# Optimization experiments

Hardware: AMD Instinct MI355X
Metric: run time of the kernel (lower is better)

The kernel has to match this reference:

```python
import jax, jax.numpy as jnp
import numpy as np

N_EDGES = 1_600_000
N_NODES = 50_000
D_FEAT = 32


def setup_inputs() -> dict:
    key = jax.random.key(0)
    k_src, k_idx = jax.random.split(key)
    src = jax.random.normal(k_src, (N_EDGES, D_FEAT), dtype=jnp.float32)
    index = jax.random.randint(k_idx, (N_EDGES,), 0, N_NODES, dtype=jnp.int64 if jax.config.jax_enable_x64 else jnp.int32)
    out = jnp.zeros((N_NODES, D_FEAT), dtype=jnp.float32)
    return {"src": src, "index": index, "out": out}


def reference(src, index, out):
    # scatter_add(src, index, dim=0, out=out): out[index[e], :] += src[e, :]
    # Equivalent to out + segment_sum over the edge dim.
    return out + jax.ops.segment_sum(src, index, num_segments=out.shape[0])
```

## Files before the change

### kernel.cpp

```cpp
#include <hip/hip_runtime.h>

#define N_EDGES 1600000
#define N_NODES 50000
#define D_FEAT  32

#define BSHIFT  6
#define NPB     64
#define NB      ((N_NODES + NPB - 1) / NPB)
#define CHUNK   4096
#define NBLK    ((N_EDGES + CHUNK - 1) / CHUNK)
#define EPT     (CHUNK / 256)

#define BLKCNT_OFF 0
#define START_OFF  ((((size_t)NBLK * NB * 4 + 255) / 256) * 256)
#define PB_OFF     (START_OFF + ((((size_t)(NB + 1) * 4 + 255) / 256) * 256))
#define OFFS_OFF   (PB_OFF + (size_t)N_EDGES * 4)
#define PERM_OFF   (OFFS_OFF + ((((size_t)(N_NODES + 1) * 4 + 255) / 256) * 256))
#define WS_NEEDED  (PERM_OFF + (size_t)N_EDGES * 4)

__global__ __launch_bounds__(256) void count_kernel(const int* __restrict__ index,
                                                    int* __restrict__ blockcnt) {
    __shared__ int lcnt[NB];
    int t = threadIdx.x;
    for (int k = t; k < NB; k += 256) lcnt[k] = 0;
    __syncthreads();
    int base = blockIdx.x * CHUNK;
    #pragma unroll
    for (int j = 0; j < EPT; ++j) {
        int e = base + j * 256 + t;
        if (e < N_EDGES) atomicAdd(&lcnt[index[e] >> BSHIFT], 1);
    }
    __syncthreads();
    for (int k = t; k < NB; k += 256)
        blockcnt[(size_t)blockIdx.x * NB + k] = lcnt[k];
}

__global__ __launch_bounds__(256) void scan_col_kernel(int* __restrict__ blockcnt,
                                                       int* __restrict__ startg) {
    int wid  = (blockIdx.x * 256 + threadIdx.x) >> 6;
    int lane = threadIdx.x & 63;
    if (wid >= NB) return;
    int carry = 0;
    const int CH = (NBLK + 63) / 64;
    for (int c = 0; c < CH; ++c) {
        int b = c * 64 + lane;
        int v = (b < NBLK) ? blockcnt[(size_t)b * NB + wid] : 0;
        int incl = v;
        #pragma unroll
        for (int d = 1; d < 64; d <<= 1) {
            int up = __shfl_up(incl, d, 64);
            if (lane >= d) incl += up;
        }
        if (b < NBLK) blockcnt[(size_t)b * NB + wid] = carry + incl - v;
        carry += __shfl(incl, 63, 64);
    }
    if (lane == 0) startg[wid] = carry;
}

__global__ __launch_bounds__(1024) void scan_bucket_kernel(int* __restrict__ startg) {
    __shared__ int part[1024];
    int t = threadIdx.x;
    int v = (t < NB) ? startg[t] : 0;
    part[t] = v;
    __syncthreads();
    int inc = v;
    for (int d = 1; d < 1024; d <<= 1) {
        int w = (t >= d) ? part[t - d] : 0;
        __syncthreads();
        inc += w;
        part[t] = inc;
        __syncthreads();
    }
    if (t < NB) startg[t] = inc - v;
    if (t == 0) startg[NB] = N_EDGES;
}

__global__ __launch_bounds__(256) void partition_kernel(const int* __restrict__ index,
                                                        const int* __restrict__ blockcnt,
                                                        const int* __restrict__ startg,
                                                        int* __restrict__ pb) {
    __shared__ int lcnt[NB];
    __shared__ int loff[NB];
    __shared__ int lbase[NB];
    __shared__ int scanp[256];
    __shared__ int2 stage[CHUNK];
    int t = threadIdx.x;
    int b = blockIdx.x;
    for (int k = t; k < NB; k += 256) lcnt[k] = 0;
    __syncthreads();
    int base = b * CHUNK;
    int nd[EPT], rk[EPT];
    #pragma unroll
    for (int j = 0; j < EPT; ++j) {
        int e = base + j * 256 + t;
        nd[j] = -1;
        if (e < N_EDGES) {
            nd[j] = index[e];
            rk[j] = atomicAdd(&lcnt[nd[j] >> BSHIFT], 1);
        }
    }
    __syncthreads();
    {
        const int C = (NB + 255) / 256;
        int mybase = t * C;
        int s = 0;
        #pragma unroll
        for (int j = 0; j < C; ++j) {
            int i = mybase + j;
            if (i < NB) s += lcnt[i];
        }
        scanp[t] = s;
        __syncthreads();
        int inc = s;
        for (int d = 1; d < 256; d <<= 1) {
            int w = (t >= d) ? scanp[t - d] : 0;
            __syncthreads();
            inc += w;
            scanp[t] = inc;
            __syncthreads();
        }
        int run = inc - s;
        #pragma unroll
        for (int j = 0; j < C; ++j) {
            int i = mybase + j;
            if (i < NB) { loff[i] = run; run += lcnt[i]; }
        }
    }
    for (int k = t; k < NB; k += 256)
        lbase[k] = startg[k] + blockcnt[(size_t)b * NB + k];
    __syncthreads();
    #pragma unroll
    for (int j = 0; j < EPT; ++j) {
        if (nd[j] >= 0) {
            int e = base + j * 256 + t;
            int k = nd[j] >> BSHIFT;
            stage[loff[k] + rk[j]] = make_int2(nd[j], e);
        }
    }
    __syncthreads();
    int total = loff[NB - 1] + lcnt[NB - 1];
    for (int i = t; i < total; i += 256) {
        int2 ent = stage[i];
        int k = ent.x >> BSHIFT;
        pb[lbase[k] + (i - loff[k])] = (ent.y << BSHIFT) | (ent.x & (NPB - 1));
    }
}

__global__ __launch_bounds__(256) void finish_kernel(const int* __restrict__ pb,
                                                     const int* __restrict__ startg,
                                                     int* __restrict__ offs,
                                                     int* __restrict__ perm) {
    __shared__ int lcnt[NPB];
    __shared__ int lcur[NPB];
    int t = threadIdx.x;
    int k = blockIdx.x;
    if (t < NPB) lcnt[t] = 0;
    __syncthreads();
    int s0 = startg[k], s1 = startg[k + 1];
    for (int i = s0 + t; i < s1; i += 256)
        atomicAdd(&lcnt[pb[i] & (NPB - 1)], 1);
    __syncthreads();
    if (t == 0) {
        int run = 0;
        for (int n = 0; n < NPB; ++n) {
            int c = lcnt[n];
            lcnt[n] = run;
            lcur[n] = run;
            run += c;
        }
    }
    __syncthreads();
    if (t < NPB) {
        int gnode = k * NPB + t;
        if (gnode < N_NODES) offs[gnode] = s0 + lcnt[t];
    }
    if (k == 0 && t == 64) offs[N_NODES] = N_EDGES;
    for (int i = s0 + t; i < s1; i += 256) {
        int pv = pb[i];
        int n = pv & (NPB - 1);
        int r = atomicAdd(&lcur[n], 1);
        perm[s0 + r] = pv >> BSHIFT;
    }
}

__global__ void gather_sum_kernel(const float4* __restrict__ src4,
                                  const int* __restrict__ perm,
                                  const int* __restrict__ offs,
                                  const float4* __restrict__ out_in4,
                                  float4* __restrict__ out4) {
    int wave = threadIdx.x >> 6;
    int node = blockIdx.x * 4 + wave;
    if (node >= N_NODES) return;
    int lane = threadIdx.x & 63;
    int slot = lane >> 3;
    int f4   = lane & 7;
    int start = offs[node];
    int end   = offs[node + 1];

    float4 a0 = {0,0,0,0}, a1 = {0,0,0,0}, a2 = {0,0,0,0}, a3 = {0,0,0,0};
    int i = start + slot;
    for (; i + 24 < end; i += 32) {
        int e0 = perm[i];
        int e1 = perm[i + 8];
        int e2 = perm[i + 16];
        int e3 = perm[i + 24];
        float4 v0 = src4[(size_t)e0 * 8 + f4];
        float4 v1 = src4[(size_t)e1 * 8 + f4];
        float4 v2 = src4[(size_t)e2 * 8 + f4];
        float4 v3 = src4[(size_t)e3 * 8 + f4];
        a0.x += v0.x; a0.y += v0.y; a0.z += v0.z; a0.w += v0.w;
        a1.x += v1.x; a1.y += v1.y; a1.z += v1.z; a1.w += v1.w;
        a2.x += v2.x; a2.y += v2.y; a2.z += v2.z; a2.w += v2.w;
        a3.x += v3.x; a3.y += v3.y; a3.z += v3.z; a3.w += v3.w;
    }
    for (; i < end; i += 8) {
        int e0 = perm[i];
        float4 v0 = src4[(size_t)e0 * 8 + f4];
        a0.x += v0.x; a0.y += v0.y; a0.z += v0.z; a0.w += v0.w;
    }
    a0.x += a1.x + a2.x + a3.x;
    a0.y += a1.y + a2.y + a3.y;
    a0.z += a1.z + a2.z + a3.z;
    a0.w += a1.w + a2.w + a3.w;

    for (int m = 8; m <= 32; m <<= 1) {
        a0.x += __shfl_xor(a0.x, m, 64);
        a0.y += __shfl_xor(a0.y, m, 64);
        a0.z += __shfl_xor(a0.z, m, 64);
        a0.w += __shfl_xor(a0.w, m, 64);
    }
    if (slot == 0) {
        size_t o = (size_t)node * 8 + f4;
        float4 b = out_in4[o];
        b.x += a0.x; b.y += a0.y; b.z += a0.z; b.w += a0.w;
        out4[o] = b;
    }
}

__global__ void init_out_kernel(const float4* __restrict__ out_in,
                                float4* __restrict__ out, int n4) {
    int i = blockIdx.x * blockDim.x + threadIdx.x;
    int stride = gridDim.x * blockDim.x;
    for (; i < n4; i += stride) out[i] = out_in[i];
}
__global__ void scatter_direct_kernel(const float* __restrict__ src,
                                      const int* __restrict__ index,
                                      float* __restrict__ out) {
    const long total = (long)N_EDGES * D_FEAT;
    long i = (long)blockIdx.x * blockDim.x + threadIdx.x;
    const long stride = (long)gridDim.x * blockDim.x;
    for (; i < total; i += stride) {
        int e = (int)(i >> 5);
        int f = (int)(i & 31);
        float v = src[i];
        int node = index[e];
        atomicAdd(&out[(size_t)node * D_FEAT + f], v);
    }
}

extern "C" void kernel_launch(void* const* d_in, const int* in_sizes, int n_in,
                              void* d_out, int out_size, void* d_ws, size_t ws_size,
                              hipStream_t stream) {
    const float* src    = (const float*)d_in[0];
    const int*   index  = (const int*)d_in[1];
    const float* out_in = (const float*)d_in[2];
    float* out          = (float*)d_out;

    if (ws_size < WS_NEEDED) {
        int n4 = out_size / 4;
        init_out_kernel<<<1563, 256, 0, stream>>>((const float4*)out_in, (float4*)out, n4);
        scatter_direct_kernel<<<2048, 256, 0, stream>>>(src, index, out);
        return;
    }

    char* ws = (char*)d_ws;
    int* blockcnt = (int*)(ws + BLKCNT_OFF);
    int* startg   = (int*)(ws + START_OFF);
    int* pb       = (int*)(ws + PB_OFF);
    int* offs     = (int*)(ws + OFFS_OFF);
    int* perm     = (int*)(ws + PERM_OFF);

    count_kernel<<<NBLK, 256, 0, stream>>>(index, blockcnt);
    scan_col_kernel<<<(NB * 64 + 255) / 256, 256, 0, stream>>>(blockcnt, startg);
    scan_bucket_kernel<<<1, 1024, 0, stream>>>(startg);
    partition_kernel<<<NBLK, 256, 0, stream>>>(index, blockcnt, startg, pb);
    finish_kernel<<<NB, 256, 0, stream>>>(pb, startg, offs, perm);
    gather_sum_kernel<<<(N_NODES + 3) / 4, 256, 0, stream>>>(
        (const float4*)src, perm, offs, (const float4*)out_in, (float4*)out);
}
```

Measured before the change: 79.62 us.

## Fuse bucket finish and gather into one kernel with shared-memory permutation

Merges the per-bucket local sort (finish) with the gather-sum, so each block builds its 64-node permutation in LDS and immediately gathers src rows for those nodes. This drops the global perm and offs arrays and one kernel launch, removing a write and re-read of 1.6M indices. It also halves CHUNK, doubling the partition and count blocks and the blockcnt matrix. Risk: the fixed LDS buffer of 6144 entries assumes no bucket exceeds that size; a larger bucket would overflow. The gather now runs on only about 782 blocks of 8 waves, which may reduce parallelism.

```diff
diff --git a/kernel.cpp b/kernel.cpp
--- a/kernel.cpp
+++ b/kernel.cpp
@@ -7,16 +7,15 @@
 #define BSHIFT  6
 #define NPB     64
 #define NB      ((N_NODES + NPB - 1) / NPB)
-#define CHUNK   4096
+#define CHUNK   2048
 #define NBLK    ((N_EDGES + CHUNK - 1) / CHUNK)
 #define EPT     (CHUNK / 256)
+#define MAXB    6144
 
 #define BLKCNT_OFF 0
 #define START_OFF  ((((size_t)NBLK * NB * 4 + 255) / 256) * 256)
 #define PB_OFF     (START_OFF + ((((size_t)(NB + 1) * 4 + 255) / 256) * 256))
-#define OFFS_OFF   (PB_OFF + (size_t)N_EDGES * 4)
-#define PERM_OFF   (OFFS_OFF + ((((size_t)(N_NODES + 1) * 4 + 255) / 256) * 256))
-#define WS_NEEDED  (PERM_OFF + (size_t)N_EDGES * 4)
+#define WS_NEEDED  (PB_OFF + (size_t)N_EDGES * 4)
 
 __global__ __launch_bounds__(256) void count_kernel(const int* __restrict__ index,
                                                     int* __restrict__ blockcnt) {
@@ -146,94 +145,84 @@
     }
 }
 
-__global__ __launch_bounds__(256) void finish_kernel(const int* __restrict__ pb,
-                                                     const int* __restrict__ startg,
-                                                     int* __restrict__ offs,
-                                                     int* __restrict__ perm) {
+__global__ __launch_bounds__(512) void finish_gather_kernel(const int* __restrict__ pb,
+                                                            const int* __restrict__ startg,
+                                                            const float4* __restrict__ src4,
+                                                            const float4* __restrict__ out_in4,
+                                                            float4* __restrict__ out4) {
+    __shared__ int lperm[MAXB];
     __shared__ int lcnt[NPB];
     __shared__ int lcur[NPB];
+    __shared__ int loffs[NPB + 1];
     int t = threadIdx.x;
     int k = blockIdx.x;
     if (t < NPB) lcnt[t] = 0;
     __syncthreads();
     int s0 = startg[k], s1 = startg[k + 1];
-    for (int i = s0 + t; i < s1; i += 256)
-        atomicAdd(&lcnt[pb[i] & (NPB - 1)], 1);
+    int cnt = s1 - s0;
+    for (int i = t; i < cnt; i += 512)
+        atomicAdd(&lcnt[pb[s0 + i] & (NPB - 1)], 1);
     __syncthreads();
     if (t == 0) {
         int run = 0;
         for (int n = 0; n < NPB; ++n) {
-            int c = lcnt[n];
-            lcnt[n] = run;
+            loffs[n] = run;
             lcur[n] = run;
-            run += c;
-        }
-    }
-    __syncthreads();
-    if (t < NPB) {
-        int gnode = k * NPB + t;
-        if (gnode < N_NODES) offs[gnode] = s0 + lcnt[t];
-    }
-    if (k == 0 && t == 64) offs[N_NODES] = N_EDGES;
-    for (int i = s0 + t; i < s1; i += 256) {
-        int pv = pb[i];
-        int n = pv & (NPB - 1);
-        int r = atomicAdd(&lcur[n], 1);
-        perm[s0 + r] = pv >> BSHIFT;
-    }
-}
-
-__global__ void gather_sum_kernel(const float4* __restrict__ src4,
-                                  const int* __restrict__ perm,
-                                  const int* __restrict__ offs,
-                                  const float4* __restrict__ out_in4,
-                                  float4* __restrict__ out4) {
-    int wave = threadIdx.x >> 6;
-    int node = blockIdx.x * 4 + wave;
-    if (node >= N_NODES) return;
-    int lane = threadIdx.x & 63;
-    int slot = lane >> 3;
-    int f4   = lane & 7;
-    int start = offs[node];
-    int end   = offs[node + 1];
-
-    float4 a0 = {0,0,0,0}, a1 = {0,0,0,0}, a2 = {0,0,0,0}, a3 = {0,0,0,0};
-    int i = start + slot;
-    for (; i + 24 < end; i += 32) {
-        int e0 = perm[i];
-        int e1 = perm[i + 8];
-        int e2 = perm[i + 16];
-        int e3 = perm[i + 24];
-        float4 v0 = src4[(size_t)e0 * 8 + f4];
-        float4 v1 = src4[(size_t)e1 * 8 + f4];
-        float4 v2 = src4[(size_t)e2 * 8 + f4];
-        float4 v3 = src4[(size_t)e3 * 8 + f4];
-        a0.x += v0.x; a0.y += v0.y; a0.z += v0.z; a0.w += v0.w;
-        a1.x += v1.x; a1.y += v1.y; a1.z += v1.z; a1.w += v1.w;
-        a2.x += v2.x; a2.y += v2.y; a2.z += v2.z; a2.w += v2.w;
-        a3.x += v3.x; a3.y += v3.y; a3.z += v3.z; a3.w += v3.w;
-    }
-    for (; i < end; i += 8) {
-        int e0 = perm[i];
-        float4 v0 = src4[(size_t)e0 * 8 + f4];
-        a0.x += v0.x; a0.y += v0.y; a0.z += v0.z; a0.w += v0.w;
-    }
-    a0.x += a1.x + a2.x + a3.x;
-    a0.y += a1.y + a2.y + a3.y;
-    a0.z += a1.z + a2.z + a3.z;
-    a0.w += a1.w + a2.w + a3.w;
-
-    for (int m = 8; m <= 32; m <<= 1) {
-        a0.x += __shfl_xor(a0.x, m, 64);
-        a0.y += __shfl_xor(a0.y, m, 64);
-        a0.z += __shfl_xor(a0.z, m, 64);
-        a0.w += __shfl_xor(a0.w, m, 64);
-    }
-    if (slot == 0) {
-        size_t o = (size_t)node * 8 + f4;
-        float4 b = out_in4[o];
-        b.x += a0.x; b.y += a0.y; b.z += a0.z; b.w += a0.w;
-        out4[o] = b;
+            run += lcnt[n];
+        }
+        loffs[NPB] = run;
+    }
+    __syncthreads();
+    for (int i = t; i < cnt; i += 512) {
+        int pv = pb[s0 + i];
+        int r = atomicAdd(&lcur[pv & (NPB - 1)], 1);
+        lperm[r] = pv >> BSHIFT;
+    }
+    __syncthreads();
+
+    int wave = t >> 6, lane = t & 63;
+    int slot = lane >> 3, f4 = lane & 7;
+    for (int nl = wave; nl < NPB; nl += 8) {
+        int gnode = k * NPB + nl;
+        if (gnode >= N_NODES) break;
+        int start = loffs[nl], end = loffs[nl + 1];
+        float4 a0 = {0,0,0,0}, a1 = {0,0,0,0}, a2 = {0,0,0,0}, a3 = {0,0,0,0};
+        int i = start + slot;
+        for (; i + 24 < end; i += 32) {
+            int e0 = lperm[i];
+            int e1 = lperm[i + 8];
+            int e2 = lperm[i + 16];
+            int e3 = lperm[i + 24];
+            float4 v0 = src4[(size_t)e0 * 8 + f4];
+            float4 v1 = src4[(size_t)e1 * 8 + f4];
+            float4 v2 = src4[(size_t)e2 * 8 + f4];
+            float4 v3 = src4[(size_t)e3 * 8 + f4];
+            a0.x += v0.x; a0.y += v0.y; a0.z += v0.z; a0.w += v0.w;
+            a1.x += v1.x; a1.y += v1.y; a1.z += v1.z; a1.w += v1.w;
+            a2.x += v2.x; a2.y += v2.y; a2.z += v2.z; a2.w += v2.w;
+            a3.x += v3.x; a3.y += v3.y; a3.z += v3.z; a3.w += v3.w;
+        }
+        for (; i < end; i += 8) {
+            int e0 = lperm[i];
+            float4 v0 = src4[(size_t)e0 * 8 + f4];
+            a0.x += v0.x; a0.y += v0.y; a0.z += v0.z; a0.w += v0.w;
+        }
+        a0.x += a1.x + a2.x + a3.x;
+        a0.y += a1.y + a2.y + a3.y;
+        a0.z += a1.z + a2.z + a3.z;
+        a0.w += a1.w + a2.w + a3.w;
+        for (int m = 8; m <= 32; m <<= 1) {
+            a0.x += __shfl_xor(a0.x, m, 64);
+            a0.y += __shfl_xor(a0.y, m, 64);
+            a0.z += __shfl_xor(a0.z, m, 64);
+            a0.w += __shfl_xor(a0.w, m, 64);
+        }
+        if (slot == 0) {
+            size_t o = (size_t)gnode * 8 + f4;
+            float4 bo = out_in4[o];
+            bo.x += a0.x; bo.y += a0.y; bo.z += a0.z; bo.w += a0.w;
+            out4[o] = bo;
+        }
     }
 }
 
@@ -277,14 +266,11 @@
     int* blockcnt = (int*)(ws + BLKCNT_OFF);
     int* startg   = (int*)(ws + START_OFF);
     int* pb       = (int*)(ws + PB_OFF);
-    int* offs     = (int*)(ws + OFFS_OFF);
-    int* perm     = (int*)(ws + PERM_OFF);
 
     count_kernel<<<NBLK, 256, 0, stream>>>(index, blockcnt);
     scan_col_kernel<<<(NB * 64 + 255) / 256, 256, 0, stream>>>(blockcnt, startg);
     scan_bucket_kernel<<<1, 1024, 0, stream>>>(startg);
     partition_kernel<<<NBLK, 256, 0, stream>>>(index, blockcnt, startg, pb);
-    finish_kernel<<<NB, 256, 0, stream>>>(pb, startg, offs, perm);
-    gather_sum_kernel<<<(N_NODES + 3) / 4, 256, 0, stream>>>(
-        (const float4*)src, perm, offs, (const float4*)out_in, (float4*)out);
-}
+    finish_gather_kernel<<<NB, 512, 0, stream>>>(pb, startg, (const float4*)src,
+                                                 (const float4*)out_in, (float4*)out);
+}
```

Result: faster. 77.22 us (-3.0%).
